# Optimization experiments

Hardware: AMD Instinct MI355X
Metric: run time of the kernel (lower is better)

Reference implementation:

```python
import jax, jax.numpy as jnp
import numpy as np

N_NODES = 4096
N_EDGES = 131072
IN_DIM = 40
HID = 128
OUT = 128
GAT_H = 2
GAT_C = 64
D_MODEL = 128
N_HEAD = 4
FF_DIM = 2048
N_LAYERS = 2
EPS = 1e-5
NEG_SLOPE = 0.2


def _layer_norm(x, g, b):
    mu = x.mean(-1, keepdims=True)
    var = ((x - mu) ** 2).mean(-1, keepdims=True)
    return (x - mu) / jnp.sqrt(var + EPS) * g + b


def _gat_conv(h, src, dst, W, a_src, a_dst, bias):
    # PyG GATConv, concat=True, eval mode (no dropout). Self loops already in (src, dst).
    N = h.shape[0]
    xw = (h @ W.T).reshape(N, GAT_H, GAT_C)          # [N, H, C]
    al_src = (xw * a_src).sum(-1)                     # [N, H]
    al_dst = (xw * a_dst).sum(-1)                     # [N, H]
    e = jax.nn.leaky_relu(al_src[src] + al_dst[dst], NEG_SLOPE)  # [E, H]
    # segment softmax over incoming edges of each dst node
    m = jax.ops.segment_max(e, dst, num_segments=N)
    ex = jnp.exp(e - m[dst])
    s = jax.ops.segment_sum(ex, dst, num_segments=N)
    alpha = ex / (s[dst] + 1e-16)                     # [E, H]
    out = jax.ops.segment_sum(xw[src] * alpha[..., None], dst, num_segments=N)
    return out.reshape(N, GAT_H * GAT_C) + bias


def _encoder_layer(x, p):
    # post-norm nn.TransformerEncoderLayer, relu FFN, eval mode
    (in_w, in_b, out_w, out_b, ln1_g, ln1_b,
     ff_w1, ff_b1, ff_w2, ff_b2, ln2_g, ln2_b) = p
    S, E = x.shape
    Dh = E // N_HEAD
    qkv = x @ in_w.T + in_b                           # [S, 3E]
    q, k, v = [t.reshape(S, N_HEAD, Dh) for t in jnp.split(qkv, 3, axis=-1)]
    scores = jnp.einsum('shd,thd->hst', q, k) / jnp.asarray(np.sqrt(Dh), x.dtype)
    attn = jax.nn.softmax(scores, axis=-1)            # [H, S, S]
    o = jnp.einsum('hst,thd->shd', attn, v).reshape(S, E) @ out_w.T + out_b
    x = _layer_norm(x + o, ln1_g, ln1_b)
    ff = jax.nn.relu(x @ ff_w1.T + ff_b1) @ ff_w2.T + ff_b2
    return _layer_norm(x + ff, ln2_g, ln2_b)


def _forward(floats, edge_index):
    (x, enc_w1, enc_b1, enc_w2, enc_b2,
     gat_w, gat_asrc, gat_adst, gat_b,
     l0_in_w, l0_in_b, l0_out_w, l0_out_b, l0_ln1_g, l0_ln1_b,
     l0_ff_w1, l0_ff_b1, l0_ff_w2, l0_ff_b2, l0_ln2_g, l0_ln2_b,
     l1_in_w, l1_in_b, l1_out_w, l1_out_b, l1_ln1_g, l1_ln1_b,
     l1_ff_w1, l1_ff_b1, l1_ff_w2, l1_ff_b2, l1_ln2_g, l1_ln2_b) = floats
    N = x.shape[0]
    # encoder MLP
    h = jax.nn.relu(x @ enc_w1.T + enc_b1) @ enc_w2.T + enc_b2
    # add one self loop per node (GATConv add_self_loops semantics)
    loop = jnp.arange(N, dtype=edge_index.dtype)
    src = jnp.concatenate([edge_index[0], loop])
    dst = jnp.concatenate([edge_index[1], loop])
    h = _gat_conv(h, src, dst, gat_w, gat_asrc, gat_adst, gat_b)
    layers = [
        (l0_in_w, l0_in_b, l0_out_w, l0_out_b, l0_ln1_g, l0_ln1_b,
         l0_ff_w1, l0_ff_b1, l0_ff_w2, l0_ff_b2, l0_ln2_g, l0_ln2_b),
        (l1_in_w, l1_in_b, l1_out_w, l1_out_b, l1_ln1_g, l1_ln1_b,
         l1_ff_w1, l1_ff_b1, l1_ff_w2, l1_ff_b2, l1_ln2_g, l1_ln2_b),
    ]
    for p in layers:
        h = _encoder_layer(h, p)
    return h


def setup_inputs() -> dict:
    key = jax.random.key(0)
    ks = jax.random.split(key, 40)
    s = 0.05
    inp = {}
    inp['x'] = jax.random.normal(ks[0], (N_NODES, IN_DIM), dtype=jnp.float32)
    # edges with src != dst (self loops added inside reference)
    src = jax.random.randint(ks[1], (N_EDGES,), 0, N_NODES)
    off = jax.random.randint(ks[2], (N_EDGES,), 1, N_NODES)
    dst = (src + off) % N_NODES
    inp['edge_index'] = jnp.stack([src, dst]).astype(jnp.int64)
    inp['enc_w1'] = jax.random.normal(ks[3], (HID, IN_DIM)) * s
    inp['enc_b1'] = jnp.zeros((HID,), jnp.float32)
    inp['enc_w2'] = jax.random.normal(ks[4], (OUT, HID)) * s
    inp['enc_b2'] = jnp.zeros((OUT,), jnp.float32)
    inp['gat_w'] = jax.random.normal(ks[5], (GAT_H * GAT_C, OUT)) * s
    inp['gat_asrc'] = jax.random.normal(ks[6], (GAT_H, GAT_C)) * s
    inp['gat_adst'] = jax.random.normal(ks[7], (GAT_H, GAT_C)) * s
    inp['gat_b'] = jnp.zeros((GAT_H * GAT_C,), jnp.float32)
    for i in range(N_LAYERS):
        k = jax.random.split(ks[8 + i], 8)
        inp[f'l{i}_in_w'] = jax.random.normal(k[0], (3 * D_MODEL, D_MODEL)) * s
        inp[f'l{i}_in_b'] = jnp.zeros((3 * D_MODEL,), jnp.float32)
        inp[f'l{i}_out_w'] = jax.random.normal(k[1], (D_MODEL, D_MODEL)) * s
        inp[f'l{i}_out_b'] = jnp.zeros((D_MODEL,), jnp.float32)
        inp[f'l{i}_ln1_g'] = jnp.ones((D_MODEL,), jnp.float32)
        inp[f'l{i}_ln1_b'] = jnp.zeros((D_MODEL,), jnp.float32)
        inp[f'l{i}_ff_w1'] = jax.random.normal(k[2], (FF_DIM, D_MODEL)) * s
        inp[f'l{i}_ff_b1'] = jnp.zeros((FF_DIM,), jnp.float32)
        inp[f'l{i}_ff_w2'] = jax.random.normal(k[3], (D_MODEL, FF_DIM)) * s
        inp[f'l{i}_ff_b2'] = jnp.zeros((D_MODEL,), jnp.float32)
        inp[f'l{i}_ln2_g'] = jnp.ones((D_MODEL,), jnp.float32)
        inp[f'l{i}_ln2_b'] = jnp.zeros((D_MODEL,), jnp.float32)
    return inp


def reference(x, edge_index, enc_w1, enc_b1, enc_w2, enc_b2,
              gat_w, gat_asrc, gat_adst, gat_b,
              l0_in_w, l0_in_b, l0_out_w, l0_out_b, l0_ln1_g, l0_ln1_b,
              l0_ff_w1, l0_ff_b1, l0_ff_w2, l0_ff_b2, l0_ln2_g, l0_ln2_b,
              l1_in_w, l1_in_b, l1_out_w, l1_out_b, l1_ln1_g, l1_ln1_b,
              l1_ff_w1, l1_ff_b1, l1_ff_w2, l1_ff_b2, l1_ln2_g, l1_ln2_b):
    floats = (x, enc_w1, enc_b1, enc_w2, enc_b2,
              gat_w, gat_asrc, gat_adst, gat_b,
              l0_in_w, l0_in_b, l0_out_w, l0_out_b, l0_ln1_g, l0_ln1_b,
              l0_ff_w1, l0_ff_b1, l0_ff_w2, l0_ff_b2, l0_ln2_g, l0_ln2_b,
              l1_in_w, l1_in_b, l1_out_w, l1_out_b, l1_ln1_g, l1_ln1_b,
              l1_ff_w1, l1_ff_b1, l1_ff_w2, l1_ff_b2, l1_ln2_g, l1_ln2_b)
    return _forward(floats, edge_index)
```

## Files before the change

### kernel.cpp

```cpp
#include <hip/hip_runtime.h>
#include <hip/hip_bf16.h>

typedef __hip_bfloat16 bf16;

#define N_NODES 4096
#define IN_DIM  40
#define DM      128
#define FF_DIM  2048
#define GAT_H   2
#define GAT_C   64
#define NHEAD   4
#define DH      32
#define LN_EPS  1e-5f
#define KSPLIT  4

typedef short s8v __attribute__((ext_vector_type(8)));
typedef float f4v __attribute__((ext_vector_type(4)));

#define WO_ENC1 0
#define WO_ENC2 8192
#define WO_GAT  24576
#define WO_L(L) (40960 + (L) * 589824)
#define WO_IN(L)  (WO_L(L))
#define WO_OUT(L) (WO_L(L) + 49152)
#define WO_FF1(L) (WO_L(L) + 65536)
#define WO_FF2(L) (WO_L(L) + 327680)
#define WBUF_ELEMS 1220608

__device__ __forceinline__ float anyload(const void* p, size_t i, int isbf) {
    if (isbf) return __bfloat162float(((const bf16*)p)[i]);
    return ((const float*)p)[i];
}
__device__ __forceinline__ int geti(const int* ei, int i, int is64) {
    return is64 ? ei[2 * (size_t)i] : ei[i];
}
__device__ __forceinline__ ushort tob(float v) {
    bf16 b = __float2bfloat16(v);
    return *(ushort*)&b;
}

__global__ void probe_kernel(const void* ones_vec, const int* ei, int* flags,
                             int* __restrict__ deg) {
    int i = blockIdx.x * 256 + threadIdx.x;
    if (i < N_NODES) deg[i] = 0;
    if (i == 0) {
        unsigned u = ((const unsigned*)ones_vec)[0];
        flags[0] = (u == 0x3F803F80u) ? 1 : 0;
        const unsigned* e = (const unsigned*)ei;
        flags[1] = (e[1] == 0u && e[3] == 0u && e[5] == 0u && e[7] == 0u) ? 1 : 0;
    }
}

__global__ __launch_bounds__(256) void wconv_kernel(const void* enc_w1, const void* enc_w2,
                                                    const void* gat_w,
                                                    const void* in_w0, const void* out_w0,
                                                    const void* ff_w10, const void* ff_w20,
                                                    const void* in_w1, const void* out_w1,
                                                    const void* ff_w11, const void* ff_w21,
                                                    ushort* __restrict__ wbuf,
                                                    const int* __restrict__ flags) {
    const int isbf = flags[0];
    int base = (blockIdx.x * 256 + threadIdx.x) * 4;
#pragma unroll
    for (int j = 0; j < 4; ++j) {
        int i = base + j;
        if (i < WO_ENC2) {
            int r = i >> 6, c = i & 63;
            float v = (c < IN_DIM) ? anyload(enc_w1, (size_t)r * IN_DIM + c, isbf) : 0.f;
            wbuf[i] = tob(v);
            continue;
        }
        const void* s;
        int si;
        if      (i < WO_GAT)     { s = enc_w2; si = i - WO_ENC2; }
        else if (i < WO_L(0))    { s = gat_w;  si = i - WO_GAT; }
        else if (i < WO_OUT(0))  { s = in_w0;  si = i - WO_IN(0); }
        else if (i < WO_FF1(0))  { s = out_w0; si = i - WO_OUT(0); }
        else if (i < WO_FF2(0))  { s = ff_w10; si = i - WO_FF1(0); }
        else if (i < WO_L(1))    { s = ff_w20; si = i - WO_FF2(0); }
        else if (i < WO_OUT(1))  { s = in_w1;  si = i - WO_IN(1); }
        else if (i < WO_FF1(1))  { s = out_w1; si = i - WO_OUT(1); }
        else if (i < WO_FF2(1))  { s = ff_w11; si = i - WO_FF1(1); }
        else                     { s = ff_w21; si = i - WO_FF2(1); }
        wbuf[i] = isbf ? ((const ushort*)s)[si] : tob(((const float*)s)[si]);
    }
}

#define K128STR 136

__global__ __launch_bounds__(256) void encgat_kernel(const void* __restrict__ X,
                                                     const void* __restrict__ b1v,
                                                     const void* __restrict__ b2v,
                                                     const ushort* __restrict__ wbuf,
                                                     const void* __restrict__ asrc,
                                                     const void* __restrict__ adst,
                                                     float* __restrict__ xwout,
                                                     float* __restrict__ als,
                                                     float* __restrict__ ald,
                                                     const int* __restrict__ flags) {
    const int isbf = flags[0];
    const int t = threadIdx.x;
    const int w = t >> 6, lane = t & 63;
    const int col = lane & 15, quad = lane >> 4;
    const int row0 = blockIdx.x * 16;
    __shared__ __align__(16) ushort As[16 * K128STR];
    __shared__ __align__(16) ushort Ws[128 * K128STR];
    __shared__ float Cs[16][132];

    {
        int r = t >> 4, c0 = (t & 15) * 4;
#pragma unroll
        for (int j = 0; j < 4; ++j) {
            int c = c0 + j;
            float v = (c < IN_DIM) ? anyload(X, (size_t)(row0 + r) * IN_DIM + c, isbf) : 0.f;
            As[r * K128STR + c] = tob(v);
        }
    }
#pragma unroll
    for (int i = 0; i < 4; ++i) {
        int idx = t + i * 256;
        int r = idx >> 3, c = (idx & 7) * 8;
        *(uint4*)&Ws[r * 72 + c] = *(const uint4*)&wbuf[WO_ENC1 + r * 64 + c];
    }
    __syncthreads();
    f4v zero = {0.f, 0.f, 0.f, 0.f};
    f4v acc1[2] = {zero, zero};
    {
        s8v a0 = *(const s8v*)&As[col * K128STR + quad * 8];
        s8v a1 = *(const s8v*)&As[col * K128STR + 32 + quad * 8];
#pragma unroll
        for (int nc = 0; nc < 2; ++nc) {
            s8v b0 = *(const s8v*)&Ws[(w * 32 + nc * 16 + col) * 72 + quad * 8];
            s8v b1 = *(const s8v*)&Ws[(w * 32 + nc * 16 + col) * 72 + 32 + quad * 8];
            acc1[nc] = __builtin_amdgcn_mfma_f32_16x16x32_bf16(a0, b0, acc1[nc], 0, 0, 0);
            acc1[nc] = __builtin_amdgcn_mfma_f32_16x16x32_bf16(a1, b1, acc1[nc], 0, 0, 0);
        }
    }
    __syncthreads();
#pragma unroll
    for (int nc = 0; nc < 2; ++nc) {
        int cc = w * 32 + nc * 16 + col;
        float bv = anyload(b1v, cc, isbf);
#pragma unroll
        for (int r = 0; r < 4; ++r)
            As[(quad * 4 + r) * K128STR + cc] = tob(fmaxf(acc1[nc][r] + bv, 0.f));
    }
#pragma unroll
    for (int i = 0; i < 8; ++i) {
        int idx = t + i * 256;
        int r = idx >> 4, c = (idx & 15) * 8;
        *(uint4*)&Ws[r * K128STR + c] = *(const uint4*)&wbuf[WO_ENC2 + r * DM + c];
    }
    __syncthreads();
    f4v acc2[2] = {zero, zero};
#pragma unroll
    for (int j = 0; j < 4; ++j) {
        s8v a = *(const s8v*)&As[col * K128STR + j * 32 + quad * 8];
#pragma unroll
        for (int nc = 0; nc < 2; ++nc) {
            s8v b = *(const s8v*)&Ws[(w * 32 + nc * 16 + col) * K128STR + j * 32 + quad * 8];
            acc2[nc] = __builtin_amdgcn_mfma_f32_16x16x32_bf16(a, b, acc2[nc], 0, 0, 0);
        }
    }
    __syncthreads();
#pragma unroll
    for (int nc = 0; nc < 2; ++nc) {
        int cc = w * 32 + nc * 16 + col;
        float bv = anyload(b2v, cc, isbf);
#pragma unroll
        for (int r = 0; r < 4; ++r)
            As[(quad * 4 + r) * K128STR + cc] = tob(acc2[nc][r] + bv);
    }
#pragma unroll
    for (int i = 0; i < 8; ++i) {
        int idx = t + i * 256;
        int r = idx >> 4, c = (idx & 15) * 8;
        *(uint4*)&Ws[r * K128STR + c] = *(const uint4*)&wbuf[WO_GAT + r * DM + c];
    }
    __syncthreads();
    f4v acc3[2] = {zero, zero};
#pragma unroll
    for (int j = 0; j < 4; ++j) {
        s8v a = *(const s8v*)&As[col * K128STR + j * 32 + quad * 8];
#pragma unroll
        for (int nc = 0; nc < 2; ++nc) {
            s8v b = *(const s8v*)&Ws[(w * 32 + nc * 16 + col) * K128STR + j * 32 + quad * 8];
            acc3[nc] = __builtin_amdgcn_mfma_f32_16x16x32_bf16(a, b, acc3[nc], 0, 0, 0);
        }
    }
#pragma unroll
    for (int nc = 0; nc < 2; ++nc) {
        int cc = w * 32 + nc * 16 + col;
#pragma unroll
        for (int r = 0; r < 4; ++r) {
            int row = quad * 4 + r;
            float v = acc3[nc][r];
            xwout[(size_t)(row0 + row) * DM + cc] = v;
            Cs[row][cc] = v;
        }
    }
    __syncthreads();
#pragma unroll
    for (int rr = 0; rr < 4; ++rr) {
        int row = w * 4 + rr;
        float x0 = Cs[row][lane], x1 = Cs[row][64 + lane];
        float s0 = x0 * anyload(asrc, lane, isbf);
        float d0 = x0 * anyload(adst, lane, isbf);
        float s1 = x1 * anyload(asrc, 64 + lane, isbf);
        float d1 = x1 * anyload(adst, 64 + lane, isbf);
#pragma unroll
        for (int o = 32; o >= 1; o >>= 1) {
            s0 += __shfl_xor(s0, o); d0 += __shfl_xor(d0, o);
            s1 += __shfl_xor(s1, o); d1 += __shfl_xor(d1, o);
        }
        if (lane == 0) {
            int n = row0 + row;
            als[n * 2 + 0] = s0; ald[n * 2 + 0] = d0;
            als[n * 2 + 1] = s1; ald[n * 2 + 1] = d1;
        }
    }
}

__global__ __launch_bounds__(256) void gemm32_kernel(const ushort* __restrict__ A,
                                                     const ushort* __restrict__ Wb,
                                                     const void* __restrict__ bias,
                                                     ushort* __restrict__ Cb,
                                                     ushort* __restrict__ vtb,
                                                     int N,
                                                     const int* __restrict__ flags,
                                                     int relu) {
    const int isbf = flags[0];
    const int t = threadIdx.x;
    const int w = t >> 6, lane = t & 63;
    const int col = lane & 15, quad = lane >> 4;
    const int wr = (w & 1) * 16, wc = (w >> 1) * 32;
    const int row0 = blockIdx.y * 32, col0 = blockIdx.x * 64;
    __shared__ __align__(16) ushort As[32 * K128STR];
    __shared__ __align__(16) ushort Ws[64 * K128STR];
#pragma unroll
    for (int i = 0; i < 2; ++i) {
        int idx = t + i * 256;
        int r = idx >> 4, c = (idx & 15) * 8;
        *(uint4*)&As[r * K128STR + c] = *(const uint4*)&A[(size_t)(row0 + r) * DM + c];
    }
#pragma unroll
    for (int i = 0; i < 4; ++i) {
        int idx = t + i * 256;
        int r = idx >> 4, c = (idx & 15) * 8;
        *(uint4*)&Ws[r * K128STR + c] = *(const uint4*)&Wb[(size_t)(col0 + r) * DM + c];
    }
    __syncthreads();
    f4v zero = {0.f, 0.f, 0.f, 0.f};
    f4v acc[2] = {zero, zero};
#pragma unroll
    for (int j = 0; j < 4; ++j) {
        s8v a = *(const s8v*)&As[(wr + col) * K128STR + j * 32 + quad * 8];
#pragma unroll
        for (int nc = 0; nc < 2; ++nc) {
            s8v b = *(const s8v*)&Ws[(wc + nc * 16 + col) * K128STR + j * 32 + quad * 8];
            acc[nc] = __builtin_amdgcn_mfma_f32_16x16x32_bf16(a, b, acc[nc], 0, 0, 0);
        }
    }
#pragma unroll
    for (int nc = 0; nc < 2; ++nc) {
        int cc = col0 + wc + nc * 16 + col;
        float bv = bias ? anyload(bias, cc, isbf) : 0.f;
#pragma unroll
        for (int r = 0; r < 4; ++r) {
            int rr = row0 + wr + quad * 4 + r;
            float v = acc[nc][r] + bv;
            if (relu) v = fmaxf(v, 0.f);
            Cb[(size_t)rr * N + cc] = tob(v);
            if (vtb && cc >= 256) vtb[(size_t)(cc - 256) * N_NODES + rr] = tob(v);
        }
    }
}

__global__ __launch_bounds__(256) void oproj_ln_kernel(const float* __restrict__ pO,
                                                       const float* __restrict__ pL,
                                                       const ushort* __restrict__ Wb,
                                                       const void* __restrict__ bias,
                                                       float* __restrict__ h,
                                                       ushort* __restrict__ hb,
                                                       const void* __restrict__ g,
                                                       const void* __restrict__ b,
                                                       const int* __restrict__ flags) {
    const int isbf = flags[0];
    const int t = threadIdx.x;
    const int w = t >> 6, lane = t & 63;
    const int col = lane & 15, quad = lane >> 4;
    const int row0 = blockIdx.x * 16;
    __shared__ __align__(16) ushort As[16 * K128STR];
    __shared__ __align__(16) ushort Ws[128 * K128STR];
    __shared__ float Cs[16][132];

    {
        int ar = t >> 4, ac = (t & 15) * 8;
        int rr = row0 + ar;
        int hh = ac >> 5, d0 = ac & 31;
        size_t qi0 = ((size_t)rr) * NHEAD + hh;
        float lsum = 0.f;
        float osum[8] = {};
#pragma unroll
        for (int kz = 0; kz < KSPLIT; ++kz) {
            size_t qi = qi0 + (size_t)kz * N_NODES * NHEAD;
            lsum += pL[qi];
            const float* po = &pO[qi * 32 + d0];
#pragma unroll
            for (int j = 0; j < 8; ++j) osum[j] += po[j];
        }
        float inv = 1.f / lsum;
#pragma unroll
        for (int j = 0; j < 8; ++j) As[ar * K128STR + ac + j] = tob(osum[j] * inv);
    }
#pragma unroll
    for (int i = 0; i < 8; ++i) {
        int idx = t + i * 256;
        int r = idx >> 4, c = (idx & 15) * 8;
        *(uint4*)&Ws[r * K128STR + c] = *(const uint4*)&Wb[(size_t)r * DM + c];
    }
    __syncthreads();
    f4v zero = {0.f, 0.f, 0.f, 0.f};
    f4v acc[2] = {zero, zero};
#pragma unroll
    for (int j = 0; j < 4; ++j) {
        s8v a = *(const s8v*)&As[col * K128STR + j * 32 + quad * 8];
#pragma unroll
        for (int nc = 0; nc < 2; ++nc) {
            s8v b = *(const s8v*)&Ws[(w * 32 + nc * 16 + col) * K128STR + j * 32 + quad * 8];
            acc[nc] = __builtin_amdgcn_mfma_f32_16x16x32_bf16(a, b, acc[nc], 0, 0, 0);
        }
    }
#pragma unroll
    for (int nc = 0; nc < 2; ++nc) {
        int cc = w * 32 + nc * 16 + col;
        float bv = bias ? anyload(bias, cc, isbf) : 0.f;
#pragma unroll
        for (int r = 0; r < 4; ++r)
            Cs[quad * 4 + r][cc] = acc[nc][r] + bv;
    }
    __syncthreads();
#pragma unroll
    for (int rr = 0; rr < 4; ++rr) {
        int row = w * 4 + rr;
        size_t base = (size_t)(row0 + row) * DM;
        float v0 = h[base + lane] + Cs[row][lane];
        float v1 = h[base + 64 + lane] + Cs[row][64 + lane];
        float s = v0 + v1;
#pragma unroll
        for (int o = 32; o >= 1; o >>= 1) s += __shfl_xor(s, o);
        float mu = s * (1.f / DM);
        float d0 = v0 - mu, d1 = v1 - mu;
        float q = d0 * d0 + d1 * d1;
#pragma unroll
        for (int o = 32; o >= 1; o >>= 1) q += __shfl_xor(q, o);
        float rstd = rsqrtf(q * (1.f / DM) + LN_EPS);
        float o0 = d0 * rstd * anyload(g, lane, isbf) + anyload(b, lane, isbf);
        float o1 = d1 * rstd * anyload(g, 64 + lane, isbf) + anyload(b, 64 + lane, isbf);
        h[base + lane] = o0;       h[base + 64 + lane] = o1;
        hb[base + lane] = tob(o0); hb[base + 64 + lane] = tob(o1);
    }
}

__global__ __launch_bounds__(512) void ff2ln_kernel(const ushort* __restrict__ A,
                                                    const ushort* __restrict__ Wb,
                                                    const void* __restrict__ fbias,
                                                    float* __restrict__ h,
                                                    ushort* __restrict__ hb,
                                                    const void* __restrict__ g,
                                                    const void* __restrict__ b,
                                                    void* __restrict__ outp,
                                                    const int* __restrict__ flags) {
    const int isbf = flags[0];
    const int t = threadIdx.x;
    const int w = t >> 6, lane = t & 63;
    const int col = lane & 15, quad = lane >> 4;
    const int row0 = blockIdx.x * 16;
    __shared__ __align__(16) ushort As[16 * K128STR];
    __shared__ __align__(16) ushort Ws[128 * K128STR];
    __shared__ float Cs[16][132];
    f4v zero = {0.f, 0.f, 0.f, 0.f};
    f4v acc = zero;
    for (int k0 = 0; k0 < FF_DIM; k0 += 128) {
        __syncthreads();
        if (t < 256) {
            int ar = t >> 4, ac = (t & 15) * 8;
            *(uint4*)&As[ar * K128STR + ac] =
                *(const uint4*)&A[(size_t)(row0 + ar) * FF_DIM + k0 + ac];
        }
#pragma unroll
        for (int i = 0; i < 4; ++i) {
            int idx = t + i * 512;
            int r = idx >> 4, c = (idx & 15) * 8;
            *(uint4*)&Ws[r * K128STR + c] = *(const uint4*)&Wb[(size_t)r * FF_DIM + k0 + c];
        }
        __syncthreads();
#pragma unroll
        for (int j = 0; j < 4; ++j) {
            s8v a = *(const s8v*)&As[col * K128STR + j * 32 + quad * 8];
            s8v bb = *(const s8v*)&Ws[(w * 16 + col) * K128STR + j * 32 + quad * 8];
            acc = __builtin_amdgcn_mfma_f32_16x16x32_bf16(a, bb, acc, 0, 0, 0);
        }
    }
    {
        int cc = w * 16 + col;
        float bv = anyload(fbias, cc, isbf);
#pragma unroll
        for (int r = 0; r < 4; ++r)
            Cs[quad * 4 + r][cc] = acc[r] + bv;
    }
    __syncthreads();
#pragma unroll
    for (int rr = 0; rr < 2; ++rr) {
        int row = w * 2 + rr;
        size_t base = (size_t)(row0 + row) * DM;
        float v0 = h[base + lane] + Cs[row][lane];
        float v1 = h[base + 64 + lane] + Cs[row][64 + lane];
        float s = v0 + v1;
#pragma unroll
        for (int o = 32; o >= 1; o >>= 1) s += __shfl_xor(s, o);
        float mu = s * (1.f / DM);
        float d0 = v0 - mu, d1 = v1 - mu;
        float q = d0 * d0 + d1 * d1;
#pragma unroll
        for (int o = 32; o >= 1; o >>= 1) q += __shfl_xor(q, o);
        float rstd = rsqrtf(q * (1.f / DM) + LN_EPS);
        float o0 = d0 * rstd * anyload(g, lane, isbf) + anyload(b, lane, isbf);
        float o1 = d1 * rstd * anyload(g, 64 + lane, isbf) + anyload(b, 64 + lane, isbf);
        h[base + lane] = o0;       h[base + 64 + lane] = o1;
        hb[base + lane] = tob(o0); hb[base + 64 + lane] = tob(o1);
        if (outp) {
            if (isbf) {
                ((ushort*)outp)[base + lane] = tob(o0);
                ((ushort*)outp)[base + 64 + lane] = tob(o1);
            } else {
                ((float*)outp)[base + lane] = o0;
                ((float*)outp)[base + 64 + lane] = o1;
            }
        }
    }
}

__global__ void deg_hist_kernel(const int* __restrict__ ei, int E0,
                                int* __restrict__ deg, const int* __restrict__ flags) {
    const int is64 = flags[1];
    int e = blockIdx.x * 256 + threadIdx.x;
    int E = E0 + N_NODES;
    if (e >= E) return;
    int d = (e < E0) ? geti(ei, E0 + e, is64) : (e - E0);
    atomicAdd(&deg[d], 1);
}

__global__ __launch_bounds__(256) void scan_kernel(const int* __restrict__ deg,
                                                   int* __restrict__ rowptr,
                                                   int* __restrict__ cursor) {
    __shared__ int part[256];
    const int t = threadIdx.x;
    const int base = t * 16;
    int loc[16];
    int s = 0;
#pragma unroll
    for (int i = 0; i < 16; ++i) { loc[i] = s; s += deg[base + i]; }
    part[t] = s;
    __syncthreads();
    for (int d = 1; d < 256; d <<= 1) {
        int v = (t >= d) ? part[t - d] : 0;
        __syncthreads();
        part[t] += v;
        __syncthreads();
    }
    int prev = (t == 0) ? 0 : part[t - 1];
#pragma unroll
    for (int i = 0; i < 16; ++i) {
        int r = prev + loc[i];
        rowptr[base + i] = r;
        cursor[base + i] = r;
    }
    if (t == 255) rowptr[N_NODES] = part[255];
}

__global__ void scatter_kernel(const int* __restrict__ ei, int E0,
                               int* __restrict__ cursor, int* __restrict__ csr_src,
                               const int* __restrict__ flags) {
    const int is64 = flags[1];
    int e = blockIdx.x * 256 + threadIdx.x;
    int E = E0 + N_NODES;
    if (e >= E) return;
    int s = (e < E0) ? geti(ei, e, is64) : (e - E0);
    int d = (e < E0) ? geti(ei, E0 + e, is64) : (e - E0);
    int pos = atomicAdd(&cursor[d], 1);
    csr_src[pos] = s;
}

__global__ __launch_bounds__(256) void gat_gather_kernel(const int* __restrict__ rowptr,
                                                         const int* __restrict__ csr_src,
                                                         const float* __restrict__ als,
                                                         const float* __restrict__ ald,
                                                         const float* __restrict__ xw,
                                                         const void* __restrict__ gat_b,
                                                         float* __restrict__ hg,
                                                         ushort* __restrict__ hgb,
                                                         const int* __restrict__ flags) {
    const int isbf = flags[0];
    const int idx = blockIdx.x * 4 + (threadIdx.x >> 6);
    const int lane = threadIdx.x & 63;
    const int d = idx >> 1, hh = idx & 1;
    const int beg = rowptr[d], end = rowptr[d + 1];
    const float aldv = ald[d * 2 + hh];

    float mx = -3.0e38f;
    for (int i = beg + lane; i < end; i += 64) {
        int s = csr_src[i];
        float v = als[s * 2 + hh] + aldv;
        v = (v > 0.f) ? v : 0.2f * v;
        mx = fmaxf(mx, v);
    }
#pragma unroll
    for (int o = 32; o >= 1; o >>= 1) mx = fmaxf(mx, __shfl_xor(mx, o));
    float sm = 0.f;
    for (int i = beg + lane; i < end; i += 64) {
        int s = csr_src[i];
        float v = als[s * 2 + hh] + aldv;
        v = (v > 0.f) ? v : 0.2f * v;
        sm += __expf(v - mx);
    }
#pragma unroll
    for (int o = 32; o >= 1; o >>= 1) sm += __shfl_xor(sm, o);
    const float inv = 1.f / (sm + 1e-16f);

    float o_acc = 0.f;
    for (int i = beg; i < end; ++i) {
        int s = csr_src[i];
        float v = als[s * 2 + hh] + aldv;
        v = (v > 0.f) ? v : 0.2f * v;
        float alpha = __expf(v - mx) * inv;
        o_acc += alpha * xw[(size_t)s * DM + hh * GAT_C + lane];
    }
    float outv = o_acc + anyload(gat_b, hh * GAT_C + lane, isbf);
    size_t off = (size_t)d * DM + hh * GAT_C + lane;
    hg[off] = outv;
    hgb[off] = tob(outv);
}

#define KSTR 40
#define VSTR 136
#define PSTR 136
__global__ __launch_bounds__(256) void attn_mfma_kernel(const ushort* __restrict__ qkvb,
                                                        const ushort* __restrict__ vtb,
                                                        float* __restrict__ pO,
                                                        float* __restrict__ pL) {
    const int hh = blockIdx.y;
    const int kz = blockIdx.z;
    const int t = threadIdx.x;
    const int w = t >> 6;
    const int lane = t & 63;
    const int col = lane & 15;
    const int quad = lane >> 4;
    const int qr = blockIdx.x * 64 + w * 16;

    __shared__ __align__(16) ushort Ks[128 * KSTR];
    __shared__ __align__(16) ushort Vt[32 * VSTR];
    __shared__ __align__(16) ushort Pl[4][16 * PSTR];

    s8v aq = *(const s8v*)&qkvb[(size_t)(qr + col) * 384 + hh * 32 + quad * 8];

    f4v zero = {0.f, 0.f, 0.f, 0.f};
    f4v of[2] = {zero, zero};
    float lacc[4] = {0.f, 0.f, 0.f, 0.f};
    const float scale = 0.17677669529663687f;
    const int k_beg = kz * (N_NODES / KSPLIT);
    const int k_end = k_beg + (N_NODES / KSPLIT);

    for (int kt = k_beg; kt < k_end; kt += 128) {
        __syncthreads();
        for (int idx = t; idx < 512; idx += 256) {
            int r = idx >> 2, c = (idx & 3) * 8;
            *(uint4*)&Ks[r * KSTR + c] =
                *(const uint4*)&qkvb[(size_t)(kt + r) * 384 + 128 + hh * 32 + c];
        }
        for (int idx = t; idx < 512; idx += 256) {
            int d = idx >> 4, c = (idx & 15) * 8;
            *(uint4*)&Vt[d * VSTR + c] =
                *(const uint4*)&vtb[(size_t)(hh * 32 + d) * N_NODES + kt + c];
        }
        __syncthreads();

        f4v sf[8];
#pragma unroll
        for (int kb = 0; kb < 8; ++kb) {
            s8v bk = *(const s8v*)&Ks[(kb * 16 + col) * KSTR + quad * 8];
            sf[kb] = __builtin_amdgcn_mfma_f32_16x16x32_bf16(aq, bk, zero, 0, 0, 0);
        }
#pragma unroll
        for (int kb = 0; kb < 8; ++kb) {
#pragma unroll
            for (int r = 0; r < 4; ++r) {
                float p = __expf(sf[kb][r] * scale);
                lacc[r] += p;
                Pl[w][(quad * 4 + r) * PSTR + kb * 16 + col] = tob(p);
            }
        }
#pragma unroll
        for (int kc = 0; kc < 4; ++kc) {
            s8v ap = *(const s8v*)&Pl[w][col * PSTR + kc * 32 + quad * 8];
#pragma unroll
            for (int nc = 0; nc < 2; ++nc) {
                s8v bv = *(const s8v*)&Vt[(nc * 16 + col) * VSTR + kc * 32 + quad * 8];
                of[nc] = __builtin_amdgcn_mfma_f32_16x16x32_bf16(ap, bv, of[nc], 0, 0, 0);
            }
        }
    }
#pragma unroll
    for (int r = 0; r < 4; ++r) {
        float lv = lacc[r];
#pragma unroll
        for (int off = 1; off <= 8; off <<= 1) lv += __shfl_xor(lv, off);
        int row = quad * 4 + r;
        size_t qi = ((size_t)kz * N_NODES + qr + row) * NHEAD + hh;
#pragma unroll
        for (int nc = 0; nc < 2; ++nc)
            pO[qi * 32 + nc * 16 + col] = of[nc][r];
        if (col == 0) pL[qi] = lv;
    }
}

extern "C" void kernel_launch(void* const* d_in, const int* in_sizes, int n_in,
                              void* d_out, int out_size, void* d_ws, size_t ws_size,
                              hipStream_t stream) {
    const void* x        = d_in[0];
    const int*  ei       = (const int*)d_in[1];
    const void* enc_w1   = d_in[2];
    const void* enc_b1   = d_in[3];
    const void* enc_w2   = d_in[4];
    const void* enc_b2   = d_in[5];
    const void* gat_w    = d_in[6];
    const void* gat_asrc = d_in[7];
    const void* gat_adst = d_in[8];
    const void* gat_b    = d_in[9];
    const void *in_w[2], *in_b[2], *out_w[2], *out_b[2], *ln1_g[2], *ln1_b[2];
    const void *ff_w1[2], *ff_b1[2], *ff_w2[2], *ff_b2[2], *ln2_g[2], *ln2_b[2];
    for (int L = 0; L < 2; ++L) {
        int base = 10 + L * 12;
        in_w[L]  = d_in[base + 0];
        in_b[L]  = d_in[base + 1];
        out_w[L] = d_in[base + 2];
        out_b[L] = d_in[base + 3];
        ln1_g[L] = d_in[base + 4];
        ln1_b[L] = d_in[base + 5];
        ff_w1[L] = d_in[base + 6];
        ff_b1[L] = d_in[base + 7];
        ff_w2[L] = d_in[base + 8];
        ff_b2[L] = d_in[base + 9];
        ln2_g[L] = d_in[base + 10];
        ln2_b[L] = d_in[base + 11];
    }
    const int E0 = in_sizes[1] / 2;
    const int E  = E0 + N_NODES;
    const size_t NN = N_NODES;

    int*    flags   = (int*)d_ws;
    float*  h       = (float*)d_ws + 64;
    ushort* hb      = (ushort*)(h + NN * DM);
    ushort* qkvb    = hb + NN * DM;
    ushort* vtb     = qkvb + NN * 384;
    ushort* ff1b    = vtb + NN * DM;
    ushort* wbuf    = ff1b + NN * FF_DIM;
    float*  pO      = (float*)(wbuf + WBUF_ELEMS);
    float*  pL      = pO + (size_t)KSPLIT * NN * NHEAD * 32;
    float*  xw      = pL + (size_t)KSPLIT * NN * NHEAD;
    float*  als     = xw + NN * DM;
    float*  ald     = als + NN * GAT_H;
    int*    deg     = (int*)(ald + NN * GAT_H);
    int*    rowptr  = deg + N_NODES;
    int*    cursor  = rowptr + N_NODES + 1;
    int*    csr_src = cursor + N_NODES;

    dim3 blk(256);

    probe_kernel<<<dim3(16), blk, 0, stream>>>(ln1_g[0], ei, flags, deg);
    wconv_kernel<<<dim3(WBUF_ELEMS / 1024), blk, 0, stream>>>(
        enc_w1, enc_w2, gat_w, in_w[0], out_w[0], ff_w1[0], ff_w2[0],
        in_w[1], out_w[1], ff_w1[1], ff_w2[1], wbuf, flags);
    deg_hist_kernel<<<dim3((E + 255) / 256), blk, 0, stream>>>(ei, E0, deg, flags);
    scan_kernel<<<dim3(1), blk, 0, stream>>>(deg, rowptr, cursor);
    scatter_kernel<<<dim3((E + 255) / 256), blk, 0, stream>>>(ei, E0, cursor, csr_src, flags);

    encgat_kernel<<<dim3(N_NODES / 16), blk, 0, stream>>>(
        x, enc_b1, enc_b2, wbuf, gat_asrc, gat_adst, xw, als, ald, flags);
    gat_gather_kernel<<<dim3(N_NODES * GAT_H / 4), blk, 0, stream>>>(
        rowptr, csr_src, als, ald, xw, gat_b, h, hb, flags);

    for (int L = 0; L < 2; ++L) {
        gemm32_kernel<<<dim3(3 * DM / 64, N_NODES / 32), blk, 0, stream>>>(
            hb, wbuf + WO_IN(L), in_b[L], qkvb, vtb, 3 * DM, flags, 0);
        attn_mfma_kernel<<<dim3(N_NODES / 64, NHEAD, KSPLIT), blk, 0, stream>>>(
            qkvb, vtb, pO, pL);
        oproj_ln_kernel<<<dim3(N_NODES / 16), blk, 0, stream>>>(
            pO, pL, wbuf + WO_OUT(L), out_b[L], h, hb, ln1_g[L], ln1_b[L], flags);
        gemm32_kernel<<<dim3(FF_DIM / 64, N_NODES / 32), blk, 0, stream>>>(
            hb, wbuf + WO_FF1(L), ff_b1[L], ff1b, nullptr, FF_DIM, flags, 1);
        ff2ln_kernel<<<dim3(N_NODES / 16), dim3(512), 0, stream>>>(
            ff1b, wbuf + WO_FF2(L), ff_b2[L], h, hb, ln2_g[L], ln2_b[L],
            (L == 1) ? d_out : nullptr, flags);
    }
}
```

Baseline: 330.4 us.

## Merge setup kernels, prefetch tiles via registers, coalesce V-transpose stores

Merges the probe and weight-conversion kernels into a single setup kernel, removing one launch. Adds register double-buffering in the FF2+LayerNorm kernel and the attention kernel, so the next K/V or weight tile loads from global memory while the current tile is computed. In the QKV GEMM, the transposed V output is staged through shared memory and written as coalesced 16-byte rows instead of scattered 2-byte stores. The cost is higher register pressure and an extra barrier pair in the GEMM epilogue.

```diff
diff --git a/kernel.cpp b/kernel.cpp
--- a/kernel.cpp
+++ b/kernel.cpp
@@ -39,31 +39,28 @@
     return *(ushort*)&b;
 }
 
-__global__ void probe_kernel(const void* ones_vec, const int* ei, int* flags,
-                             int* __restrict__ deg) {
-    int i = blockIdx.x * 256 + threadIdx.x;
-    if (i < N_NODES) deg[i] = 0;
-    if (i == 0) {
-        unsigned u = ((const unsigned*)ones_vec)[0];
-        flags[0] = (u == 0x3F803F80u) ? 1 : 0;
-        const unsigned* e = (const unsigned*)ei;
-        flags[1] = (e[1] == 0u && e[3] == 0u && e[5] == 0u && e[7] == 0u) ? 1 : 0;
-    }
-}
-
-__global__ __launch_bounds__(256) void wconv_kernel(const void* enc_w1, const void* enc_w2,
+__global__ __launch_bounds__(256) void setup_kernel(const void* ones_vec, const int* ei,
+                                                    int* flags, int* __restrict__ deg,
+                                                    const void* enc_w1, const void* enc_w2,
                                                     const void* gat_w,
                                                     const void* in_w0, const void* out_w0,
                                                     const void* ff_w10, const void* ff_w20,
                                                     const void* in_w1, const void* out_w1,
                                                     const void* ff_w11, const void* ff_w21,
-                                                    ushort* __restrict__ wbuf,
-                                                    const int* __restrict__ flags) {
-    const int isbf = flags[0];
-    int base = (blockIdx.x * 256 + threadIdx.x) * 4;
+                                                    ushort* __restrict__ wbuf) {
+    const int isbf = (((const unsigned*)ones_vec)[0] == 0x3F803F80u) ? 1 : 0;
+    int gid = blockIdx.x * 256 + threadIdx.x;
+    if (gid < N_NODES) deg[gid] = 0;
+    if (gid == 0) {
+        flags[0] = isbf;
+        const unsigned* e = (const unsigned*)ei;
+        flags[1] = (e[1] == 0u && e[3] == 0u && e[5] == 0u && e[7] == 0u) ? 1 : 0;
+    }
+    int base = gid * 4;
 #pragma unroll
     for (int j = 0; j < 4; ++j) {
         int i = base + j;
+        if (i >= WBUF_ELEMS) break;
         if (i < WO_ENC2) {
             int r = i >> 6, c = i & 63;
             float v = (c < IN_DIM) ? anyload(enc_w1, (size_t)r * IN_DIM + c, isbf) : 0.f;
@@ -261,6 +258,8 @@
             acc[nc] = __builtin_amdgcn_mfma_f32_16x16x32_bf16(a, b, acc[nc], 0, 0, 0);
         }
     }
+    const int vpath = (vtb != nullptr) && (col0 >= 256);
+    ushort vloc[2][4];
 #pragma unroll
     for (int nc = 0; nc < 2; ++nc) {
         int cc = col0 + wc + nc * 16 + col;
@@ -270,9 +269,24 @@
             int rr = row0 + wr + quad * 4 + r;
             float v = acc[nc][r] + bv;
             if (relu) v = fmaxf(v, 0.f);
-            Cb[(size_t)rr * N + cc] = tob(v);
-            if (vtb && cc >= 256) vtb[(size_t)(cc - 256) * N_NODES + rr] = tob(v);
-        }
+            ushort hv = tob(v);
+            Cb[(size_t)rr * N + cc] = hv;
+            vloc[nc][r] = hv;
+        }
+    }
+    if (vpath) {
+        __syncthreads();
+#pragma unroll
+        for (int nc = 0; nc < 2; ++nc) {
+            int lc = wc + nc * 16 + col;
+#pragma unroll
+            for (int r = 0; r < 4; ++r)
+                As[lc * 40 + wr + quad * 4 + r] = vloc[nc][r];
+        }
+        __syncthreads();
+        int d = t >> 2, seg = t & 3;
+        *(uint4*)&vtb[(size_t)(col0 - 256 + d) * N_NODES + row0 + seg * 8] =
+            *(const uint4*)&As[d * 40 + seg * 8];
     }
 }
 
@@ -381,20 +395,32 @@
     __shared__ float Cs[16][132];
     f4v zero = {0.f, 0.f, 0.f, 0.f};
     f4v acc = zero;
-    for (int k0 = 0; k0 < FF_DIM; k0 += 128) {
+
+    const int wrr[4] = { (t) >> 4, (t + 512) >> 4, (t + 1024) >> 4, (t + 1536) >> 4 };
+    const int wcc = (t & 15) * 8;
+    const int ar = t >> 4, ac = (t & 15) * 8;
+
+    uint4 wreg[4];
+    uint4 areg = {};
+#pragma unroll
+    for (int i = 0; i < 4; ++i)
+        wreg[i] = *(const uint4*)&Wb[(size_t)wrr[i] * FF_DIM + wcc];
+    if (t < 256) areg = *(const uint4*)&A[(size_t)(row0 + ar) * FF_DIM + ac];
+
+    for (int it = 0; it < 16; ++it) {
         __syncthreads();
-        if (t < 256) {
-            int ar = t >> 4, ac = (t & 15) * 8;
-            *(uint4*)&As[ar * K128STR + ac] =
-                *(const uint4*)&A[(size_t)(row0 + ar) * FF_DIM + k0 + ac];
-        }
-#pragma unroll
-        for (int i = 0; i < 4; ++i) {
-            int idx = t + i * 512;
-            int r = idx >> 4, c = (idx & 15) * 8;
-            *(uint4*)&Ws[r * K128STR + c] = *(const uint4*)&Wb[(size_t)r * FF_DIM + k0 + c];
-        }
+        if (t < 256) *(uint4*)&As[ar * K128STR + ac] = areg;
+#pragma unroll
+        for (int i = 0; i < 4; ++i)
+            *(uint4*)&Ws[wrr[i] * K128STR + wcc] = wreg[i];
         __syncthreads();
+        if (it < 15) {
+            int k0 = (it + 1) * 128;
+#pragma unroll
+            for (int i = 0; i < 4; ++i)
+                wreg[i] = *(const uint4*)&Wb[(size_t)wrr[i] * FF_DIM + k0 + wcc];
+            if (t < 256) areg = *(const uint4*)&A[(size_t)(row0 + ar) * FF_DIM + k0 + ac];
+        }
 #pragma unroll
         for (int j = 0; j < 4; ++j) {
             s8v a = *(const s8v*)&As[col * K128STR + j * 32 + quad * 8];
@@ -571,19 +597,34 @@
     const int k_beg = kz * (N_NODES / KSPLIT);
     const int k_end = k_beg + (N_NODES / KSPLIT);
 
+    const int kr0 = t >> 2,        kc0 = (t & 3) * 8;
+    const int kr1 = (t >> 2) + 64;
+    const int vd0 = t >> 4,        vc0 = (t & 15) * 8;
+    const int vd1 = (t >> 4) + 16;
+
+    uint4 kreg0, kreg1, vreg0, vreg1;
+    {
+        int kt = k_beg;
+        kreg0 = *(const uint4*)&qkvb[(size_t)(kt + kr0) * 384 + 128 + hh * 32 + kc0];
+        kreg1 = *(const uint4*)&qkvb[(size_t)(kt + kr1) * 384 + 128 + hh * 32 + kc0];
+        vreg0 = *(const uint4*)&vtb[(size_t)(hh * 32 + vd0) * N_NODES + kt + vc0];
+        vreg1 = *(const uint4*)&vtb[(size_t)(hh * 32 + vd1) * N_NODES + kt + vc0];
+    }
+
     for (int kt = k_beg; kt < k_end; kt += 128) {
         __syncthreads();
-        for (int idx = t; idx < 512; idx += 256) {
-            int r = idx >> 2, c = (idx & 3) * 8;
-            *(uint4*)&Ks[r * KSTR + c] =
-                *(const uint4*)&qkvb[(size_t)(kt + r) * 384 + 128 + hh * 32 + c];
-        }
-        for (int idx = t; idx < 512; idx += 256) {
-            int d = idx >> 4, c = (idx & 15) * 8;
-            *(uint4*)&Vt[d * VSTR + c] =
-                *(const uint4*)&vtb[(size_t)(hh * 32 + d) * N_NODES + kt + c];
-        }
+        *(uint4*)&Ks[kr0 * KSTR + kc0] = kreg0;
+        *(uint4*)&Ks[kr1 * KSTR + kc0] = kreg1;
+        *(uint4*)&Vt[vd0 * VSTR + vc0] = vreg0;
+        *(uint4*)&Vt[vd1 * VSTR + vc0] = vreg1;
         __syncthreads();
+        if (kt + 128 < k_end) {
+            int kn = kt + 128;
+            kreg0 = *(const uint4*)&qkvb[(size_t)(kn + kr0) * 384 + 128 + hh * 32 + kc0];
+            kreg1 = *(const uint4*)&qkvb[(size_t)(kn + kr1) * 384 + 128 + hh * 32 + kc0];
+            vreg0 = *(const uint4*)&vtb[(size_t)(hh * 32 + vd0) * N_NODES + kn + vc0];
+            vreg1 = *(const uint4*)&vtb[(size_t)(hh * 32 + vd1) * N_NODES + kn + vc0];
+        }
 
         f4v sf[8];
 #pragma unroll
@@ -677,10 +718,10 @@
 
     dim3 blk(256);
 
-    probe_kernel<<<dim3(16), blk, 0, stream>>>(ln1_g[0], ei, flags, deg);
-    wconv_kernel<<<dim3(WBUF_ELEMS / 1024), blk, 0, stream>>>(
+    setup_kernel<<<dim3((WBUF_ELEMS + 1023) / 1024), blk, 0, stream>>>(
+        ln1_g[0], ei, flags, deg,
         enc_w1, enc_w2, gat_w, in_w[0], out_w[0], ff_w1[0], ff_w2[0],
-        in_w[1], out_w[1], ff_w1[1], ff_w2[1], wbuf, flags);
+        in_w[1], out_w[1], ff_w1[1], ff_w2[1], wbuf);
     deg_hist_kernel<<<dim3((E + 255) / 256), blk, 0, stream>>>(ei, E0, deg, flags);
     scan_kernel<<<dim3(1), blk, 0, stream>>>(deg, rowptr, cursor);
     scatter_kernel<<<dim3((E + 255) / 256), blk, 0, stream>>>(ei, E0, cursor, csr_src, flags);
```

After: 363.9 us. 1.1x slower.
